# Performance work log

Hardware: AMD Instinct MI355X
Metric: run time of the kernel (lower is better)

Reference implementation:

```python
import jax, jax.numpy as jnp
import numpy as np

N_NODES = 100000


def gcn_layer(x, row, col, ew, W, b, n_nodes):
    # PyG GCNConv: add self-loops (weight 1), symmetric normalization
    # deg^{-1/2}[row] * w * deg^{-1/2}[col], linear transform, scatter-add to col.
    loop = jnp.arange(n_nodes, dtype=row.dtype)
    row_f = jnp.concatenate([row, loop])
    col_f = jnp.concatenate([col, loop])
    ew_f = jnp.concatenate([ew, jnp.ones((n_nodes,), dtype=ew.dtype)])
    deg = jax.ops.segment_sum(ew_f, col_f, num_segments=n_nodes)  # [N]
    dinv = jnp.where(deg > 0, jax.lax.rsqrt(deg), 0.0)
    norm = dinv[row_f] * ew_f * dinv[col_f]  # [E+N]
    h = x @ W  # [N, F_out]
    msg = norm[:, None] * h[row_f]  # [E+N, F_out]
    out = jax.ops.segment_sum(msg, col_f, num_segments=n_nodes)
    return out + b


def setup_inputs() -> dict:
    key = jax.random.key(0)
    ks = jax.random.split(key, 6)
    n, e, d_in, d_h = N_NODES, 3200000, 128, 16
    x = jax.random.normal(ks[0], (n, d_in), dtype=jnp.float32)
    edge_index = jax.random.randint(ks[1], (2, e), 0, n, dtype=jnp.int64)
    edge_weight = jax.random.uniform(ks[2], (e,), dtype=jnp.float32)
    W1 = jax.random.normal(ks[3], (d_in, d_h), dtype=jnp.float32) * (1.0 / np.sqrt(d_in))
    b1 = jnp.zeros((d_h,), dtype=jnp.float32)
    W2 = jax.random.normal(ks[4], (d_h, 1), dtype=jnp.float32) * (1.0 / np.sqrt(d_h))
    b2 = jnp.zeros((1,), dtype=jnp.float32)
    return {"x": x, "edge_index": edge_index, "edge_weight": edge_weight,
            "W1": W1, "b1": b1, "W2": W2, "b2": b2}


def reference(x, edge_index, edge_weight, W1, b1, W2, b2):
    row, col = edge_index[0], edge_index[1]
    n = x.shape[0]
    h = gcn_layer(x, row, col, edge_weight, W1, b1, n)
    h = jax.nn.relu(h)
    out = gcn_layer(h, row, col, edge_weight, W2, b2, n)
    return out.squeeze(-1)  # [N]
```

## Files before the change

### kernel.cpp

```cpp
#include <hip/hip_runtime.h>
#include <hip/hip_bf16.h>


#define DH 16
#define BSH 6
#define BNODES 64
#define NB_MAX 1568
#define CHUNK 4096
#define HCHUNK 8192
#define NSLICE 4
#define SE_CAP 768
#define CH2 1024

#define BFL(u) __uint_as_float((u) << 16)
#define BFH(u) __uint_as_float((u) & 0xFFFF0000u)

typedef unsigned int u32x2 __attribute__((ext_vector_type(2)));

static __device__ __forceinline__ uint2 ntload_u2(const uint2* p) {
    u32x2 v = __builtin_nontemporal_load((const u32x2*)p);
    return make_uint2(v.x, v.y);
}

__global__ __launch_bounds__(256) void k_hist2(const int* __restrict__ row,
                                               const int* __restrict__ col,
                                               int* __restrict__ gCnt,
                                               int* __restrict__ rCnt, int E, int NB) {
    __shared__ int lc[NB_MAX];
    __shared__ int lr[NB_MAX];
    const int tid = threadIdx.x;
    for (int i = tid; i < NB; i += 256) { lc[i] = 0; lr[i] = 0; }
    __syncthreads();
    const int base = blockIdx.x * HCHUNK;
    #pragma unroll
    for (int k = 0; k < 32; ++k) {
        int e = base + tid + 256 * k;
        if (e < E) {
            atomicAdd(&lc[col[e] >> BSH], 1);
            atomicAdd(&lr[row[e] >> BSH], 1);
        }
    }
    __syncthreads();
    for (int i = tid; i < NB; i += 256) {
        if (lc[i]) atomicAdd(&gCnt[i], lc[i]);
        if (lr[i]) atomicAdd(&rCnt[i], lr[i]);
    }
}

__global__ __launch_bounds__(1024) void k_Ascan(const int* __restrict__ cnt,
                                                int* __restrict__ basep,
                                                int* __restrict__ cursor,
                                                int NB, int E) {
    __shared__ int s[1024];
    const int t = threadIdx.x;
    const int i0 = 2 * t, i1 = 2 * t + 1;
    int a = (i0 < NB) ? cnt[i0] : 0;
    int b = (i1 < NB) ? cnt[i1] : 0;
    int v = a + b;
    s[t] = v;
    __syncthreads();
    for (int off = 1; off < 1024; off <<= 1) {
        int u = (t >= off) ? s[t - off] : 0;
        __syncthreads();
        s[t] += u;
        __syncthreads();
    }
    int ex = s[t] - v;
    if (i0 < NB) { basep[i0] = ex;     cursor[i0] = ex; }
    if (i1 < NB) { basep[i1] = ex + a; cursor[i1] = ex + a; }
    if (t == 0) basep[NB] = E;
}

__global__ __launch_bounds__(256) void k_Ascatter(const int* __restrict__ row,
                                                  const int* __restrict__ col,
                                                  const float* __restrict__ ew,
                                                  int* __restrict__ gCursor,
                                                  uint2* __restrict__ edata,
                                                  int* __restrict__ pos,
                                                  int E, int NB) {
    __shared__ int lh[NB_MAX];
    __shared__ int lbase[NB_MAX];
    __shared__ int lcur[NB_MAX];
    __shared__ int tsum[256];
    __shared__ unsigned short sbuck[CHUNK];
    __shared__ uint2 stage[CHUNK];
    const int tid = threadIdx.x;
    for (int i = tid; i < NB; i += 256) lh[i] = 0;
    __syncthreads();
    const int base = blockIdx.x * CHUNK;
    int r_[16], c_[16];
    float w_[16];
    #pragma unroll
    for (int k = 0; k < 16; ++k) {
        int e = base + tid + 256 * k;
        bool ok = e < E;
        c_[k] = ok ? col[e] : -1;
        r_[k] = ok ? row[e] : 0;
        w_[k] = ok ? ew[e] : 0.f;
        if (ok) atomicAdd(&lh[c_[k] >> BSH], 1);
    }
    __syncthreads();
    const int t0 = tid * 8;
    int c8[8];
    int mysum = 0;
    #pragma unroll
    for (int k = 0; k < 8; ++k) {
        c8[k] = (t0 + k < NB) ? lh[t0 + k] : 0;
        mysum += c8[k];
    }
    tsum[tid] = mysum;
    __syncthreads();
    for (int off = 1; off < 256; off <<= 1) {
        int u = (tid >= off) ? tsum[tid - off] : 0;
        __syncthreads();
        tsum[tid] += u;
        __syncthreads();
    }
    int p = tsum[tid] - mysum;
    #pragma unroll
    for (int k = 0; k < 8; ++k) {
        if (t0 + k < NB) { lbase[t0 + k] = p; lcur[t0 + k] = p; }
        p += c8[k];
    }
    __syncthreads();
    for (int b = tid; b < NB; b += 256) {
        int cnt = lh[b];
        if (cnt) {
            int g = atomicAdd(&gCursor[b], cnt);
            lh[b] = g - lbase[b];
        }
    }
    __syncthreads();
    #pragma unroll
    for (int k = 0; k < 16; ++k) {
        if (c_[k] >= 0) {
            int b = c_[k] >> BSH;
            unsigned rem = (unsigned)(c_[k] & (BNODES - 1));
            int sp = atomicAdd(&lcur[b], 1);
            stage[sp] = make_uint2((unsigned)r_[k] | (rem << 20), __float_as_uint(w_[k]));
            sbuck[sp] = (unsigned short)b;
            pos[base + tid + 256 * k] = lh[b] + sp;
        }
    }
    __syncthreads();
    int nE = E - base;
    if (nE > CHUNK) nE = CHUNK;
    for (int j = tid; j < nE; j += 256)
        edata[lh[sbuck[j]] + j] = stage[j];
}

__global__ __launch_bounds__(256) void k_Rscatter(const int* __restrict__ row,
                                                  const int* __restrict__ pos,
                                                  int* __restrict__ rCursor,
                                                  uint* __restrict__ rrec,
                                                  int E, int NB) {
    __shared__ int lh[NB_MAX];
    __shared__ int lbase[NB_MAX];
    __shared__ int lcur[NB_MAX];
    __shared__ int tsum[256];
    __shared__ unsigned short sbuck[CHUNK];
    __shared__ uint stage[CHUNK];
    const int tid = threadIdx.x;
    for (int i = tid; i < NB; i += 256) lh[i] = 0;
    __syncthreads();
    const int base = blockIdx.x * CHUNK;
    int r_[16];
    uint p_[16];
    #pragma unroll
    for (int k = 0; k < 16; ++k) {
        int e = base + tid + 256 * k;
        bool ok = e < E;
        r_[k] = ok ? row[e] : -1;
        p_[k] = ok ? (uint)pos[e] : 0u;
        if (ok) atomicAdd(&lh[r_[k] >> BSH], 1);
    }
    __syncthreads();
    const int t0 = tid * 8;
    int c8[8];
    int mysum = 0;
    #pragma unroll
    for (int k = 0; k < 8; ++k) {
        c8[k] = (t0 + k < NB) ? lh[t0 + k] : 0;
        mysum += c8[k];
    }
    tsum[tid] = mysum;
    __syncthreads();
    for (int off = 1; off < 256; off <<= 1) {
        int u = (tid >= off) ? tsum[tid - off] : 0;
        __syncthreads();
        tsum[tid] += u;
        __syncthreads();
    }
    int p = tsum[tid] - mysum;
    #pragma unroll
    for (int k = 0; k < 8; ++k) {
        if (t0 + k < NB) { lbase[t0 + k] = p; lcur[t0 + k] = p; }
        p += c8[k];
    }
    __syncthreads();
    for (int bb = tid; bb < NB; bb += 256) {
        int cnt = lh[bb];
        if (cnt) {
            int g = atomicAdd(&rCursor[bb], cnt);
            lh[bb] = g - lbase[bb];
        }
    }
    __syncthreads();
    #pragma unroll
    for (int k = 0; k < 16; ++k) {
        if (r_[k] >= 0) {
            int bb = r_[k] >> BSH;
            uint rem = (uint)(r_[k] & (BNODES - 1));
            int sp = atomicAdd(&lcur[bb], 1);
            stage[sp] = p_[k] | (rem << 26);
            sbuck[sp] = (unsigned short)bb;
        }
    }
    __syncthreads();
    int nE = E - base;
    if (nE > CHUNK) nE = CHUNK;
    for (int j = tid; j < nE; j += 256)
        rrec[lh[sbuck[j]] + j] = stage[j];
}

__global__ __launch_bounds__(256) void k_deg(const int* __restrict__ gBase,
                                             const uint2* __restrict__ edata,
                                             float* __restrict__ deg, int N) {
    __shared__ float dg[BNODES];
    const int tid = threadIdx.x;
    if (tid < BNODES) dg[tid] = 0.f;
    __syncthreads();
    const int b = blockIdx.x;
    const int s = gBase[b], e = gBase[b + 1];
    for (int i = s + blockIdx.y * 256 + tid; i < e; i += 512) {
        uint2 ed = ntload_u2(&edata[i]);
        atomicAdd(&dg[ed.x >> 20], __uint_as_float(ed.y));
    }
    __syncthreads();
    int node = (b << BSH) + tid;
    if (tid < BNODES && node < N && dg[tid] != 0.f)
        atomicAdd(&deg[node], dg[tid]);
}

__global__ __launch_bounds__(256) void k_h1(const float* __restrict__ x,
                                            const float* __restrict__ W1,
                                            const float* __restrict__ deg,
                                            float* __restrict__ dinv,
                                            __hip_bfloat16* __restrict__ hdb) {
    __shared__ float Ws[128 * DH];
    __shared__ float xs[16 * 132];
    const int t = threadIdx.x;
    const int node0 = blockIdx.x * 16;
    #pragma unroll
    for (int i = 0; i < 8; ++i) Ws[t + 256 * i] = W1[t + 256 * i];
    const float4* xg = (const float4*)(x + (size_t)node0 * 128);
    #pragma unroll
    for (int it = 0; it < 2; ++it) {
        int idx = t + 256 * it;
        int n = idx >> 5, k4 = idx & 31;
        float4 v = xg[n * 32 + k4];
        *(float4*)(&xs[n * 132 + k4 * 4]) = v;
    }
    __syncthreads();
    const int node = t >> 4, feat = t & 15;
    const float* xr = &xs[node * 132];
    float acc = 0.f;
    #pragma unroll 8
    for (int k = 0; k < 128; ++k) acc += xr[k] * Ws[k * DH + feat];
    const int v = node0 + node;
    const float di = rsqrtf(deg[v] + 1.0f);
    if (feat == 0) dinv[v] = di;
    hdb[(size_t)v * DH + feat] = __float2bfloat16(di * acc);
}

__global__ __launch_bounds__(256) void k_gather1(
    const int* __restrict__ gBase, const uint2* __restrict__ edata,
    const __hip_bfloat16* __restrict__ hdb, float* __restrict__ partial) {
    __shared__ float acc[BNODES][DH + 1];
    __shared__ uint2 se[SE_CAP];
    const int tid = threadIdx.x;
    for (int i = tid; i < BNODES * (DH + 1); i += 256) ((float*)acc)[i] = 0.f;
    const int b = blockIdx.x, sl = blockIdx.y;
    const int s = gBase[b], e = gBase[b + 1];
    const int L = e - s;
    const int per = (L + NSLICE - 1) / NSLICE;
    const int s0 = s + sl * per;
    const int e0 = (s0 + per < e) ? (s0 + per) : e;
    const int g = tid >> 3;
    const int f2 = tid & 7;
    const uint* __restrict__ hp = (const uint*)hdb;

    for (int c0 = s0; c0 < e0; c0 += SE_CAP) {
        const int len = ((e0 - c0) < SE_CAP) ? (e0 - c0) : SE_CAP;
        __syncthreads();
        for (int j = tid; j < len; j += 256) se[j] = ntload_u2(&edata[c0 + j]);
        __syncthreads();
        const int nfull = len & ~255;
        for (int j0 = 0; j0 < nfull; j0 += 256) {
            uint2 ed[8];
            uint hv[8];
            #pragma unroll
            for (int k = 0; k < 8; ++k) ed[k] = se[j0 + g + k * 32];
            #pragma unroll
            for (int k = 0; k < 8; ++k)
                hv[k] = hp[(size_t)(ed[k].x & 0xFFFFFu) * 8 + f2];
            #pragma unroll
            for (int k = 0; k < 8; ++k) {
                const float w = __uint_as_float(ed[k].y);
                const int rem = ed[k].x >> 20;
                atomicAdd(&acc[rem][2 * f2],     w * BFL(hv[k]));
                atomicAdd(&acc[rem][2 * f2 + 1], w * BFH(hv[k]));
            }
        }
        for (int j = nfull + g; j < len; j += 32) {
            const uint2 ed = se[j];
            const uint hv = hp[(size_t)(ed.x & 0xFFFFFu) * 8 + f2];
            const float w = __uint_as_float(ed.y);
            const int rem = ed.x >> 20;
            atomicAdd(&acc[rem][2 * f2],     w * BFL(hv));
            atomicAdd(&acc[rem][2 * f2 + 1], w * BFH(hv));
        }
    }
    __syncthreads();
    float* ps = partial + ((size_t)b * NSLICE + sl) * (DH * BNODES);
    for (int i = tid; i < DH * BNODES; i += 256)
        ps[i] = acc[i >> 4][i & 15];
}

__global__ __launch_bounds__(256) void k_fin1q(
    const float* __restrict__ partial, const float* __restrict__ dinv,
    const __hip_bfloat16* __restrict__ hdb, const float* __restrict__ b1,
    const float* __restrict__ W2, const float* __restrict__ b2,
    const int* __restrict__ rBase, const uint* __restrict__ rrec,
    __hip_bfloat16* __restrict__ qe, float* __restrict__ out, int N) {
    __shared__ float acc[BNODES][DH + 1];
    __shared__ float b1s[DH], W2s[DH];
    __shared__ __hip_bfloat16 qls[BNODES];
    const int tid = threadIdx.x;
    if (tid < DH) { b1s[tid] = b1[tid]; W2s[tid] = W2[tid]; }
    const int b = blockIdx.x;
    const float* ps = partial + (size_t)b * NSLICE * (DH * BNODES);
    for (int i = tid; i < DH * BNODES; i += 256) {
        float s = 0.f;
        #pragma unroll
        for (int sl = 0; sl < NSLICE; ++sl) s += ps[sl * (DH * BNODES) + i];
        acc[i >> 4][i & 15] = s;
    }
    __syncthreads();
    int node = (b << BSH) + tid;
    if (tid < BNODES && node < N) {
        float dc = dinv[node];
        const __hip_bfloat16* hs = hdb + (size_t)node * DH;
        float t = 0.f;
        #pragma unroll
        for (int f = 0; f < DH; ++f) {
            float hv = __bfloat162float(hs[f]);
            t += fmaxf(dc * (acc[tid][f] + hv) + b1s[f], 0.f) * W2s[f];
        }
        float qq = dc * t;
        qls[tid] = __float2bfloat16(qq);
        out[node] = b2[0] + dc * qq;
    } else if (tid < BNODES) {
        qls[tid] = __float2bfloat16(0.f);
    }
    __syncthreads();
    const int r0 = rBase[b], r1 = rBase[b + 1];
    for (int j = r0 + tid; j < r1; j += 256) {
        uint rec = rrec[j];
        qe[rec & 0x03FFFFFFu] = qls[rec >> 26];
    }
}

__global__ __launch_bounds__(256) void k_gather2q(
    const int* __restrict__ gBase, const uint2* __restrict__ edata,
    const float* __restrict__ dinv, const __hip_bfloat16* __restrict__ qe,
    float* __restrict__ out, int N) {
    __shared__ float a2[BNODES];
    __shared__ uint2 se[CH2];
    __shared__ ushort sq[CH2];
    const int tid = threadIdx.x;
    if (tid < BNODES) a2[tid] = 0.f;
    const int b = blockIdx.x;
    const int s = gBase[b], e = gBase[b + 1];
    const int L = e - s;
    const int per = (L + 1) >> 1;
    const int s0 = s + blockIdx.y * per;
    const int e0 = (s0 + per < e) ? (s0 + per) : e;
    const ushort* __restrict__ qp = (const ushort*)qe;

    for (int c0 = s0; c0 < e0; c0 += CH2) {
        const int len = ((e0 - c0) < CH2) ? (e0 - c0) : CH2;
        __syncthreads();
        for (int i = tid; i < len; i += 256) se[i] = ntload_u2(&edata[c0 + i]);
        for (int i = tid; i < len; i += 256) sq[i] = qp[c0 + i];
        __syncthreads();
        #pragma unroll
        for (int k = 0; k < CH2 / 256; ++k) {
            const int idx = tid + k * 256;
            if (idx < len) {
                const uint2 d = se[idx];
                const float q = __uint_as_float((uint)sq[idx] << 16);
                atomicAdd(&a2[d.x >> 20], __uint_as_float(d.y) * q);
            }
        }
    }
    __syncthreads();
    int node = (b << BSH) + tid;
    if (tid < BNODES && node < N && a2[tid] != 0.f)
        atomicAdd(&out[node], dinv[node] * a2[tid]);
}

extern "C" void kernel_launch(void* const* d_in, const int* in_sizes, int n_in,
                              void* d_out, int out_size, void* d_ws, size_t ws_size,
                              hipStream_t stream) {
    const float* x  = (const float*)d_in[0];
    const int*   ei = (const int*)d_in[1];
    const float* ew = (const float*)d_in[2];
    const float* W1 = (const float*)d_in[3];
    const float* b1 = (const float*)d_in[4];
    const float* W2 = (const float*)d_in[5];
    const float* b2 = (const float*)d_in[6];
    float* out = (float*)d_out;

    const int N = in_sizes[0] / 128;
    const int E = in_sizes[2];
    const int* row = ei;
    const int* col = ei + E;
    const int NB = (N + BNODES - 1) >> BSH;
    const int NBp = NB_MAX;

    const int hblocks = (E + HCHUNK - 1) / HCHUNK;
    const int sblocks = (E + CHUNK - 1) / CHUNK;

    char* base = (char*)d_ws;
    size_t off = 0;
    #define ALLOC(ptr_t, name, bytes) \
        ptr_t name = (ptr_t)(base + off); off = (off + (size_t)(bytes) + 255) & ~(size_t)255;
    ALLOC(int*,   gCnt,    (size_t)NBp * 4)
    ALLOC(int*,   rCnt,    (size_t)NBp * 4)
    ALLOC(float*, deg,     (size_t)N * 4)
    ALLOC(int*,   gBase,   (size_t)NBp * 4)
    ALLOC(int*,   rBase,   (size_t)NBp * 4)
    ALLOC(int*,   gCursor, (size_t)NBp * 4)
    ALLOC(int*,   rCursor, (size_t)NBp * 4)
    ALLOC(float*, dinv,    (size_t)N * 4)
    ALLOC(__hip_bfloat16*, hdb, (size_t)16 * N * 2)
    ALLOC(__hip_bfloat16*, qe,  (size_t)E * 2)
    ALLOC(int*,   pos,     (size_t)E * 4)
    ALLOC(uint*,  rrec,    (size_t)E * 4)
    ALLOC(float*, partial, (size_t)NB * NSLICE * (DH * BNODES) * 4)
    ALLOC(uint2*, edata,   (size_t)E * 8)
    #undef ALLOC

    hipMemsetAsync(gCnt, 0, ((size_t)NBp) * sizeof(int), stream);
    hipMemsetAsync(rCnt, 0, ((size_t)NBp) * sizeof(int), stream);
    hipMemsetAsync(deg,  0, ((size_t)N) * sizeof(float), stream);
    k_hist2<<<hblocks, 256, 0, stream>>>(row, col, gCnt, rCnt, E, NB);
    k_Ascan<<<1, 1024, 0, stream>>>(gCnt, gBase, gCursor, NB, E);
    k_Ascan<<<1, 1024, 0, stream>>>(rCnt, rBase, rCursor, NB, E);
    k_Ascatter<<<sblocks, 256, 0, stream>>>(row, col, ew, gCursor, edata, pos, E, NB);
    k_Rscatter<<<sblocks, 256, 0, stream>>>(row, pos, rCursor, rrec, E, NB);
    k_deg<<<dim3(NB, 2), 256, 0, stream>>>(gBase, edata, deg, N);
    k_h1<<<N / 16, 256, 0, stream>>>(x, W1, deg, dinv, hdb);
    k_gather1<<<dim3(NB, NSLICE), 256, 0, stream>>>(gBase, edata, hdb, partial);
    k_fin1q<<<NB, 256, 0, stream>>>(partial, dinv, hdb, b1, W2, b2,
                                    rBase, rrec, qe, out, N);
    k_gather2q<<<dim3(NB, 2), 256, 0, stream>>>(gBase, edata, dinv, qe, out, N);
}
```

Baseline: 635.2 us.

## Replace per-edge q scatter with source-sorted edge copy and push-style layer-2 scatter

Layer 2 no longer writes a per-edge bf16 q array through a pos/rrec permutation. A second edge copy sorted by source node (rdata holding col, row remainder and weight) is built instead. Layer 2 reads q per source block from shared memory and atomically adds into a global per-node buffer, and a small final kernel applies dinv and the bias. This removes the pos and rrec arrays and the random per-edge q writes, but adds an 8-byte-per-edge scatter and random global float atomics on o2.

```diff
diff --git a/kernel.cpp b/kernel.cpp
--- a/kernel.cpp
+++ b/kernel.cpp
@@ -76,7 +76,6 @@
                                                   const float* __restrict__ ew,
                                                   int* __restrict__ gCursor,
                                                   uint2* __restrict__ edata,
-                                                  int* __restrict__ pos,
                                                   int E, int NB) {
     __shared__ int lh[NB_MAX];
     __shared__ int lbase[NB_MAX];
@@ -139,7 +138,6 @@
             int sp = atomicAdd(&lcur[b], 1);
             stage[sp] = make_uint2((unsigned)r_[k] | (rem << 20), __float_as_uint(w_[k]));
             sbuck[sp] = (unsigned short)b;
-            pos[base + tid + 256 * k] = lh[b] + sp;
         }
     }
     __syncthreads();
@@ -149,29 +147,31 @@
         edata[lh[sbuck[j]] + j] = stage[j];
 }
 
-__global__ __launch_bounds__(256) void k_Rscatter(const int* __restrict__ row,
-                                                  const int* __restrict__ pos,
-                                                  int* __restrict__ rCursor,
-                                                  uint* __restrict__ rrec,
-                                                  int E, int NB) {
+__global__ __launch_bounds__(256) void k_Rscatter2(const int* __restrict__ row,
+                                                   const int* __restrict__ col,
+                                                   const float* __restrict__ ew,
+                                                   int* __restrict__ rCursor,
+                                                   uint2* __restrict__ rdata,
+                                                   int E, int NB) {
     __shared__ int lh[NB_MAX];
     __shared__ int lbase[NB_MAX];
     __shared__ int lcur[NB_MAX];
     __shared__ int tsum[256];
     __shared__ unsigned short sbuck[CHUNK];
-    __shared__ uint stage[CHUNK];
+    __shared__ uint2 stage[CHUNK];
     const int tid = threadIdx.x;
     for (int i = tid; i < NB; i += 256) lh[i] = 0;
     __syncthreads();
     const int base = blockIdx.x * CHUNK;
-    int r_[16];
-    uint p_[16];
+    int r_[16], c_[16];
+    float w_[16];
     #pragma unroll
     for (int k = 0; k < 16; ++k) {
         int e = base + tid + 256 * k;
         bool ok = e < E;
         r_[k] = ok ? row[e] : -1;
-        p_[k] = ok ? (uint)pos[e] : 0u;
+        c_[k] = ok ? col[e] : 0;
+        w_[k] = ok ? ew[e] : 0.f;
         if (ok) atomicAdd(&lh[r_[k] >> BSH], 1);
     }
     __syncthreads();
@@ -210,9 +210,9 @@
     for (int k = 0; k < 16; ++k) {
         if (r_[k] >= 0) {
             int bb = r_[k] >> BSH;
-            uint rem = (uint)(r_[k] & (BNODES - 1));
+            uint rrem = (uint)(r_[k] & (BNODES - 1));
             int sp = atomicAdd(&lcur[bb], 1);
-            stage[sp] = p_[k] | (rem << 26);
+            stage[sp] = make_uint2((uint)c_[k] | (rrem << 20), __float_as_uint(w_[k]));
             sbuck[sp] = (unsigned short)bb;
         }
     }
@@ -220,7 +220,7 @@
     int nE = E - base;
     if (nE > CHUNK) nE = CHUNK;
     for (int j = tid; j < nE; j += 256)
-        rrec[lh[sbuck[j]] + j] = stage[j];
+        rdata[lh[sbuck[j]] + j] = stage[j];
 }
 
 __global__ __launch_bounds__(256) void k_deg(const int* __restrict__ gBase,
@@ -327,15 +327,13 @@
         ps[i] = acc[i >> 4][i & 15];
 }
 
-__global__ __launch_bounds__(256) void k_fin1q(
+__global__ __launch_bounds__(256) void k_fin1b(
     const float* __restrict__ partial, const float* __restrict__ dinv,
     const __hip_bfloat16* __restrict__ hdb, const float* __restrict__ b1,
-    const float* __restrict__ W2, const float* __restrict__ b2,
-    const int* __restrict__ rBase, const uint* __restrict__ rrec,
-    __hip_bfloat16* __restrict__ qe, float* __restrict__ out, int N) {
+    const float* __restrict__ W2,
+    float* __restrict__ qb, int N) {
     __shared__ float acc[BNODES][DH + 1];
     __shared__ float b1s[DH], W2s[DH];
-    __shared__ __hip_bfloat16 qls[BNODES];
     const int tid = threadIdx.x;
     if (tid < DH) { b1s[tid] = b1[tid]; W2s[tid] = W2[tid]; }
     const int b = blockIdx.x;
@@ -357,57 +355,50 @@
             float hv = __bfloat162float(hs[f]);
             t += fmaxf(dc * (acc[tid][f] + hv) + b1s[f], 0.f) * W2s[f];
         }
-        float qq = dc * t;
-        qls[tid] = __float2bfloat16(qq);
-        out[node] = b2[0] + dc * qq;
-    } else if (tid < BNODES) {
-        qls[tid] = __float2bfloat16(0.f);
-    }
-    __syncthreads();
-    const int r0 = rBase[b], r1 = rBase[b + 1];
-    for (int j = r0 + tid; j < r1; j += 256) {
-        uint rec = rrec[j];
-        qe[rec & 0x03FFFFFFu] = qls[rec >> 26];
-    }
-}
-
-__global__ __launch_bounds__(256) void k_gather2q(
-    const int* __restrict__ gBase, const uint2* __restrict__ edata,
-    const float* __restrict__ dinv, const __hip_bfloat16* __restrict__ qe,
-    float* __restrict__ out, int N) {
-    __shared__ float a2[BNODES];
+        qb[node] = dc * t;
+    }
+}
+
+__global__ __launch_bounds__(256) void k_gather2s(
+    const int* __restrict__ rBase, const uint2* __restrict__ rdata,
+    const float* __restrict__ qb, float* __restrict__ o2, int N) {
+    __shared__ float qls[BNODES];
     __shared__ uint2 se[CH2];
-    __shared__ ushort sq[CH2];
-    const int tid = threadIdx.x;
-    if (tid < BNODES) a2[tid] = 0.f;
+    const int tid = threadIdx.x;
+    if (tid < BNODES) {
+        int node = (blockIdx.x << BSH) + tid;
+        qls[tid] = (node < N) ? qb[node] : 0.f;
+    }
     const int b = blockIdx.x;
-    const int s = gBase[b], e = gBase[b + 1];
+    const int s = rBase[b], e = rBase[b + 1];
     const int L = e - s;
     const int per = (L + 1) >> 1;
     const int s0 = s + blockIdx.y * per;
     const int e0 = (s0 + per < e) ? (s0 + per) : e;
-    const ushort* __restrict__ qp = (const ushort*)qe;
 
     for (int c0 = s0; c0 < e0; c0 += CH2) {
         const int len = ((e0 - c0) < CH2) ? (e0 - c0) : CH2;
         __syncthreads();
-        for (int i = tid; i < len; i += 256) se[i] = ntload_u2(&edata[c0 + i]);
-        for (int i = tid; i < len; i += 256) sq[i] = qp[c0 + i];
+        for (int i = tid; i < len; i += 256) se[i] = ntload_u2(&rdata[c0 + i]);
         __syncthreads();
         #pragma unroll
         for (int k = 0; k < CH2 / 256; ++k) {
             const int idx = tid + k * 256;
             if (idx < len) {
-                const uint2 d = se[idx];
-                const float q = __uint_as_float((uint)sq[idx] << 16);
-                atomicAdd(&a2[d.x >> 20], __uint_as_float(d.y) * q);
+                const uint2 ed = se[idx];
+                const float v = __uint_as_float(ed.y) * qls[ed.x >> 20];
+                if (v != 0.f) atomicAdd(&o2[ed.x & 0xFFFFFu], v);
             }
         }
     }
-    __syncthreads();
-    int node = (b << BSH) + tid;
-    if (tid < BNODES && node < N && a2[tid] != 0.f)
-        atomicAdd(&out[node], dinv[node] * a2[tid]);
+}
+
+__global__ __launch_bounds__(256) void k_fin2(
+    const float* __restrict__ qb, const float* __restrict__ o2,
+    const float* __restrict__ dinv, const float* __restrict__ b2,
+    float* __restrict__ out, int N) {
+    int n = blockIdx.x * 256 + threadIdx.x;
+    if (n < N) out[n] = b2[0] + dinv[n] * (qb[n] + o2[n]);
 }
 
 extern "C" void kernel_launch(void* const* d_in, const int* in_sizes, int n_in,
@@ -445,25 +436,26 @@
     ALLOC(int*,   rCursor, (size_t)NBp * 4)
     ALLOC(float*, dinv,    (size_t)N * 4)
     ALLOC(__hip_bfloat16*, hdb, (size_t)16 * N * 2)
-    ALLOC(__hip_bfloat16*, qe,  (size_t)E * 2)
-    ALLOC(int*,   pos,     (size_t)E * 4)
-    ALLOC(uint*,  rrec,    (size_t)E * 4)
+    ALLOC(float*, qb,      (size_t)N * 4)
+    ALLOC(float*, o2,      (size_t)N * 4)
     ALLOC(float*, partial, (size_t)NB * NSLICE * (DH * BNODES) * 4)
     ALLOC(uint2*, edata,   (size_t)E * 8)
+    ALLOC(uint2*, rdata,   (size_t)E * 8)
     #undef ALLOC
 
-    hipMemsetAsync(gCnt, 0, ((size_t)NBp) * sizeof(int), stream);
-    hipMemsetAsync(rCnt, 0, ((size_t)NBp) * sizeof(int), stream);
-    hipMemsetAsync(deg,  0, ((size_t)N) * sizeof(float), stream);
+    hipMemsetAsync(gCnt, 0, (size_t)NBp * sizeof(int), stream);
+    hipMemsetAsync(rCnt, 0, (size_t)NBp * sizeof(int), stream);
+    hipMemsetAsync(deg,  0, (size_t)N * sizeof(float), stream);
+    hipMemsetAsync(o2,   0, (size_t)N * sizeof(float), stream);
     k_hist2<<<hblocks, 256, 0, stream>>>(row, col, gCnt, rCnt, E, NB);
     k_Ascan<<<1, 1024, 0, stream>>>(gCnt, gBase, gCursor, NB, E);
     k_Ascan<<<1, 1024, 0, stream>>>(rCnt, rBase, rCursor, NB, E);
-    k_Ascatter<<<sblocks, 256, 0, stream>>>(row, col, ew, gCursor, edata, pos, E, NB);
-    k_Rscatter<<<sblocks, 256, 0, stream>>>(row, pos, rCursor, rrec, E, NB);
+    k_Ascatter<<<sblocks, 256, 0, stream>>>(row, col, ew, gCursor, edata, E, NB);
+    k_Rscatter2<<<sblocks, 256, 0, stream>>>(row, col, ew, rCursor, rdata, E, NB);
     k_deg<<<dim3(NB, 2), 256, 0, stream>>>(gBase, edata, deg, N);
     k_h1<<<N / 16, 256, 0, stream>>>(x, W1, deg, dinv, hdb);
     k_gather1<<<dim3(NB, NSLICE), 256, 0, stream>>>(gBase, edata, hdb, partial);
-    k_fin1q<<<NB, 256, 0, stream>>>(partial, dinv, hdb, b1, W2, b2,
-                                    rBase, rrec, qe, out, N);
-    k_gather2q<<<dim3(NB, 2), 256, 0, stream>>>(gBase, edata, dinv, qe, out, N);
-}
+    k_fin1b<<<NB, 256, 0, stream>>>(partial, dinv, hdb, b1, W2, qb, N);
+    k_gather2s<<<dim3(NB, 2), 256, 0, stream>>>(rBase, rdata, qb, o2, N);
+    k_fin2<<<(N + 255) / 256, 256, 0, stream>>>(qb, o2, dinv, b2, out, N);
+}
```

Result: slower. 723.0 us (+13.8%).
